# Performance work log

Measured on AMD Instinct MI355X. Metric: run time of the kernel, lower is better.

## Reference

```python
import jax, jax.numpy as jnp
import numpy as np

D_MODEL = 1024
N_HEADS = 16
DIM_HEAD = D_MODEL // N_HEADS
SCALE = DIM_HEAD ** (-0.5)
B, T = 8, 1024


def setup_inputs() -> dict:
    key = jax.random.key(0)
    k1, k2, k3 = jax.random.split(key, 3)
    x = jax.random.normal(k1, (B, T, D_MODEL), dtype=jnp.float32)
    m = jnp.ones((B, T), dtype=jnp.float32)  # padding mask (1 = keep)
    w_qkv = jax.random.normal(k2, (3 * D_MODEL, D_MODEL), dtype=jnp.float32) * (D_MODEL ** -0.5)
    w_out = jax.random.normal(k3, (D_MODEL, D_MODEL), dtype=jnp.float32) * (D_MODEL ** -0.5)
    b_out = jnp.zeros((D_MODEL,), dtype=jnp.float32)
    return {"x": x, "m": m, "w_qkv": w_qkv, "w_out": w_out, "b_out": b_out, "l": T}


def reference(x, m, w_qkv, w_out, b_out, l):
    b, t, dm = x.shape
    qkv = jnp.einsum('btd,ed->bte', x, w_qkv)  # (b,t,3*d_model)
    q, k, v = jnp.split(qkv, 3, axis=-1)
    rs = lambda a: a.reshape(b, t, N_HEADS, DIM_HEAD)
    q, k, v = rs(q), rs(k), rs(v)
    e = jnp.einsum('bihd,bjhd->bijh', q, k) * SCALE  # (b,i,j,h)
    # combined padding + causal mask
    kpm = m[:, :, None] * m[:, None, :]              # (b,i,j)
    kpm = jnp.tril(kpm)[..., None]                   # (b,i,j,1)
    neg = -jnp.finfo(e.dtype).max
    e = jnp.where(kpm == 0, neg, e)
    a = jax.nn.softmax(e, axis=2)                    # softmax over j
    o = jnp.einsum('bijh,bjhd->bihd', a, v).reshape(b, t, dm)
    o = jnp.einsum('btd,ed->bte', o, w_out) + b_out
    # dropout is identity in eval mode
    return o * m[..., None]
```

## Files before the change

### kernel.cpp

```cpp
#include <hip/hip_runtime.h>
#include <cstdint>
#include <cstddef>

typedef unsigned short u16;
typedef __bf16 bf16;
typedef bf16 __attribute__((ext_vector_type(2))) bf16x2;
typedef bf16 __attribute__((ext_vector_type(4))) bf16x4;
typedef bf16 __attribute__((ext_vector_type(8))) bf16x8;
typedef float __attribute__((ext_vector_type(4))) f32x4;
typedef u16 __attribute__((ext_vector_type(8))) u16x8;

#define QSCALE 0.18033688011112042f

__device__ __forceinline__ u16 f2b(float x) {
  unsigned u = __float_as_uint(x);
  unsigned r = (u + 0x7fffu + ((u >> 16) & 1u)) >> 16;
  return (u16)r;
}

__device__ __forceinline__ void gl_lds16(const void* g, void* lds) {
  __builtin_amdgcn_global_load_lds(
      (const __attribute__((address_space(1))) unsigned int*)g,
      (__attribute__((address_space(3))) unsigned int*)lds, 16, 0, 0);
}

__device__ __forceinline__ bf16x8 frag(const u16* base, int row, int kchunk) {
  const int c = kchunk ^ (row & 7);
  return *(const bf16x8*)(base + row * 64 + c * 8);
}
__device__ __forceinline__ void stage_tile4(const u16* gbase, int K, char* lbase,
                                            int wave, int lane) {
#pragma unroll
  for (int i = 0; i < 4; ++i) {
    const int q = wave * 64 + lane + i * 256;
    const int r = q >> 3, c = (q & 7) ^ (r & 7);
    gl_lds16(gbase + (size_t)r * K + c * 8, lbase + i * 4096 + wave * 1024);
  }
}

__device__ __forceinline__ bf16x8 frag32(const u16* base, int row, int kchunk) {
  const int c = kchunk ^ ((row >> 1) & 3);
  return *(const bf16x8*)(base + row * 32 + c * 8);
}
__device__ __forceinline__ void stage32(const u16* gbase, int K, char* lbase,
                                        int wave, int lane) {
  const int q0 = wave * 64 + lane;
  const int r0 = q0 >> 2, c0 = (q0 & 3) ^ ((r0 >> 1) & 3);
  gl_lds16(gbase + (size_t)r0 * K + c0 * 8, lbase + wave * 1024);
  const int q1 = q0 + 256;
  const int r1 = q1 >> 2, c1 = (q1 & 3) ^ ((r1 >> 1) & 3);
  gl_lds16(gbase + (size_t)r1 * K + c1 * 8, lbase + 4096 + wave * 1024);
}

__global__ __launch_bounds__(256) void castk(const float* __restrict__ in,
                                             u16* __restrict__ out, int n) {
  int i = (blockIdx.x * 256 + threadIdx.x) * 8;
  if (i >= n) return;
  float4 a = *(const float4*)(in + i);
  float4 b = *(const float4*)(in + i + 4);
  u16x8 v;
  v[0] = f2b(a.x); v[1] = f2b(a.y); v[2] = f2b(a.z); v[3] = f2b(a.w);
  v[4] = f2b(b.x); v[5] = f2b(b.y); v[6] = f2b(b.z); v[7] = f2b(b.w);
  *(u16x8*)(out + i) = v;
}

__global__ __launch_bounds__(256, 4) void gemm_qkv(
    const u16* __restrict__ A, const u16* __restrict__ B,
    u16* __restrict__ Qo, u16* __restrict__ Ko, u16* __restrict__ Vo) {
  __shared__ u16 As[2][128 * 32];
  __shared__ u16 Bs[2][128 * 32];
  const int tid = threadIdx.x;
  const int lane = tid & 63, wave = tid >> 6;
  const int fr = lane & 15, fg = lane >> 4;
  const int wr = wave >> 1, wc = wave & 1;
  const int bid = blockIdx.x;
  const int bm = bid & 63, bn = bid >> 6;
  const int K = 1024;
  const u16* Ab = A + (size_t)bm * 128 * K;
  const u16* Bb = B + (size_t)bn * 128 * K;

  f32x4 acc[4][4] = {};

  stage32(Ab, K, (char*)&As[0][0], wave, lane);
  stage32(Bb, K, (char*)&Bs[0][0], wave, lane);
  __syncthreads();

  int cur = 0;
#pragma unroll 1
  for (int t = 0; t < 32; ++t) {
    if (t < 31) {
      stage32(Ab + (size_t)(t + 1) * 32, K, (char*)&As[cur ^ 1][0], wave, lane);
      stage32(Bb + (size_t)(t + 1) * 32, K, (char*)&Bs[cur ^ 1][0], wave, lane);
    }
    bf16x8 af[4], bfv[4];
#pragma unroll
    for (int mi = 0; mi < 4; ++mi)
      af[mi] = frag32(&As[cur][0], wr * 64 + mi * 16 + fr, fg);
#pragma unroll
    for (int ni = 0; ni < 4; ++ni)
      bfv[ni] = frag32(&Bs[cur][0], wc * 64 + ni * 16 + fr, fg);
#pragma unroll
    for (int mi = 0; mi < 4; ++mi)
#pragma unroll
      for (int ni = 0; ni < 4; ++ni)
        acc[mi][ni] = __builtin_amdgcn_mfma_f32_16x16x32_bf16(
            af[mi], bfv[ni], acc[mi][ni], 0, 0, 0);
    __syncthreads();
    cur ^= 1;
  }

  const int gr0 = bm * 128 + wr * 64;
  const int gc0 = bn * 128 + wc * 64;
#pragma unroll
  for (int mi = 0; mi < 4; ++mi) {
    const int rb = gr0 + mi * 16 + fg * 4;
    const int b = rb >> 10, t = rb & 1023;
#pragma unroll
    for (int ni = 0; ni < 4; ++ni) {
      const int c = gc0 + ni * 16 + fr;
      const int region = c >> 10, cc = c & 1023;
      const int h = cc >> 6, d = cc & 63;
      const size_t bh = (size_t)(b * 16 + h);
      if (region == 0) {
#pragma unroll
        for (int g = 0; g < 4; ++g)
          Qo[(bh * 1024 + t + g) * 64 + d] = f2b(acc[mi][ni][g] * QSCALE);
      } else if (region == 1) {
#pragma unroll
        for (int g = 0; g < 4; ++g)
          Ko[(bh * 1024 + t + g) * 64 + d] = f2b(acc[mi][ni][g]);
      } else {
        ushort4 pv;
        pv.x = f2b(acc[mi][ni][0]);
        pv.y = f2b(acc[mi][ni][1]);
        pv.z = f2b(acc[mi][ni][2]);
        pv.w = f2b(acc[mi][ni][3]);
        *(ushort4*)(Vo + (bh * 64 + d) * 1024 + t) = pv;
      }
    }
  }
}

__global__ __launch_bounds__(256) void gemm_bt2(
    const u16* __restrict__ A, const u16* __restrict__ B,
    float* __restrict__ Co, const float* __restrict__ bias,
    const float* __restrict__ msk) {
  __shared__ u16 As[2][128 * 64];
  __shared__ u16 Bs[2][128 * 64];
  const int tid = threadIdx.x;
  const int lane = tid & 63, wave = tid >> 6;
  const int fr = lane & 15, fg = lane >> 4;
  const int wr = wave >> 1, wc = wave & 1;
  const int bid = blockIdx.x;
  const int bm = bid & 63, bn = bid >> 6;
  const int K = 1024, N = 1024;
  const u16* Ab = A + (size_t)bm * 128 * K;
  const u16* Bb = B + (size_t)bn * 128 * K;

  f32x4 acc[4][4] = {};

  stage_tile4(Ab, K, (char*)&As[0][0], wave, lane);
  stage_tile4(Bb, K, (char*)&Bs[0][0], wave, lane);
  __syncthreads();

  int cur = 0;
#pragma unroll 1
  for (int t = 0; t < 16; ++t) {
    if (t < 15) {
      stage_tile4(Ab + (size_t)(t + 1) * 64, K, (char*)&As[cur ^ 1][0], wave, lane);
      stage_tile4(Bb + (size_t)(t + 1) * 64, K, (char*)&Bs[cur ^ 1][0], wave, lane);
    }
    bf16x8 af[4][2], bfv[4][2];
#pragma unroll
    for (int mi = 0; mi < 4; ++mi)
#pragma unroll
      for (int kk = 0; kk < 2; ++kk)
        af[mi][kk] = frag(&As[cur][0], wr * 64 + mi * 16 + fr, kk * 4 + fg);
#pragma unroll
    for (int ni = 0; ni < 4; ++ni)
#pragma unroll
      for (int kk = 0; kk < 2; ++kk)
        bfv[ni][kk] = frag(&Bs[cur][0], wc * 64 + ni * 16 + fr, kk * 4 + fg);
#pragma unroll
    for (int mi = 0; mi < 4; ++mi)
#pragma unroll
      for (int ni = 0; ni < 4; ++ni)
#pragma unroll
        for (int kk = 0; kk < 2; ++kk)
          acc[mi][ni] = __builtin_amdgcn_mfma_f32_16x16x32_bf16(
              af[mi][kk], bfv[ni][kk], acc[mi][ni], 0, 0, 0);
    __syncthreads();
    cur ^= 1;
  }

  const int gr0 = bm * 128 + wr * 64;
  const int gc0 = bn * 128 + wc * 64;
#pragma unroll
  for (int mi = 0; mi < 4; ++mi) {
    const int rb = gr0 + mi * 16 + fg * 4;
#pragma unroll
    for (int ni = 0; ni < 4; ++ni) {
      const int c = gc0 + ni * 16 + fr;
      const float bo = bias[c];
#pragma unroll
      for (int g = 0; g < 4; ++g) {
        const int r = rb + g;
        Co[(size_t)r * N + c] = (acc[mi][ni][g] + bo) * msk[r];
      }
    }
  }
}

__global__ __launch_bounds__(256) void attnk(const u16* __restrict__ Qb,
                                             const u16* __restrict__ Kb,
                                             const u16* __restrict__ Vtb,
                                             const float* __restrict__ msk,
                                             u16* __restrict__ Ob) {
  __shared__ u16 Ks[2][64 * 64];
  __shared__ u16 Vs[2][64 * 64];
  const int tid = threadIdx.x;
  const int lane = tid & 63, wave = tid >> 6;
  const int fr = lane & 15, fg = lane >> 4;
  const int bid = blockIdx.x;
  __constant__ static const int tab[8] = {7, 6, 0, 1, 5, 4, 2, 3};
  const int qi = tab[bid >> 7];
  const int bh = bid & 127;
  const int b = bh >> 4, h = bh & 15;
  const int qw = qi * 128 + wave * 32;

  bf16x8 qf[2][2];
#pragma unroll
  for (int ct = 0; ct < 2; ++ct)
#pragma unroll
    for (int kc = 0; kc < 2; ++kc)
      qf[ct][kc] = *(const bf16x8*)(Qb + ((size_t)bh * 1024 + qw + ct * 16 + fr) * 64 +
                                    kc * 32 + fg * 8);

  f32x4 o[2][4] = {};
  float mrun[2], lrun[2];
  mrun[0] = mrun[1] = -3.0e38f;
  lrun[0] = lrun[1] = 0.f;

  const int src0 = fr + ((fg & 1) << 5);
  const int src1 = src0 + 16;

  const int cc0 = wave * 64 + lane;
  const int krow0 = cc0 >> 3, kcb0 = (cc0 & 7) ^ (krow0 & 7);
  const int cc1 = 256 + cc0;
  const int krow1 = cc1 >> 3, kcb1 = (cc1 & 7) ^ (krow1 & 7);

  const int nkb = qi * 2 + 2;

  gl_lds16(Kb + ((size_t)bh * 1024 + krow0) * 64 + kcb0 * 8, (char*)&Ks[0][0] + wave * 1024);
  gl_lds16(Vtb + ((size_t)bh * 64 + krow0) * 1024 + kcb0 * 8, (char*)&Vs[0][0] + wave * 1024);
  gl_lds16(Kb + ((size_t)bh * 1024 + krow1) * 64 + kcb1 * 8, (char*)&Ks[0][0] + 4096 + wave * 1024);
  gl_lds16(Vtb + ((size_t)bh * 64 + krow1) * 1024 + kcb1 * 8, (char*)&Vs[0][0] + 4096 + wave * 1024);

#pragma unroll 1
  for (int kb = 0; kb < nkb; ++kb) {
    __syncthreads();
    if (kb + 1 < nkb) {
      char* kd = (char*)&Ks[(kb + 1) & 1][0];
      char* vd = (char*)&Vs[(kb + 1) & 1][0];
      gl_lds16(Kb + ((size_t)bh * 1024 + (kb + 1) * 64 + krow0) * 64 + kcb0 * 8, kd + wave * 1024);
      gl_lds16(Vtb + ((size_t)bh * 64 + krow0) * 1024 + (kb + 1) * 64 + kcb0 * 8, vd + wave * 1024);
      gl_lds16(Kb + ((size_t)bh * 1024 + (kb + 1) * 64 + krow1) * 64 + kcb1 * 8, kd + 4096 + wave * 1024);
      gl_lds16(Vtb + ((size_t)bh * 64 + krow1) * 1024 + (kb + 1) * 64 + kcb1 * 8, vd + 4096 + wave * 1024);
    }
    if (kb * 64 > qw + 31) continue;
    const u16* Kc = &Ks[kb & 1][0];
    const u16* Vc = &Vs[kb & 1][0];

    f32x4 st[2][4];
    const f32x4 z = {0.f, 0.f, 0.f, 0.f};
#pragma unroll
    for (int nt = 0; nt < 4; ++nt) {
      const int krow = nt * 16 + fr;
      const int cb0r = (0 * 4 + fg) ^ (krow & 7);
      const int cb1r = (1 * 4 + fg) ^ (krow & 7);
      const bf16x8 kf0 = *(const bf16x8*)(Kc + krow * 64 + cb0r * 8);
      const bf16x8 kf1 = *(const bf16x8*)(Kc + krow * 64 + cb1r * 8);
#pragma unroll
      for (int ct = 0; ct < 2; ++ct) {
        st[ct][nt] = __builtin_amdgcn_mfma_f32_16x16x32_bf16(kf0, qf[ct][0], z, 0, 0, 0);
        st[ct][nt] = __builtin_amdgcn_mfma_f32_16x16x32_bf16(kf1, qf[ct][1], st[ct][nt], 0, 0, 0);
      }
    }

    float kmv[4][4];
#pragma unroll
    for (int nt = 0; nt < 4; ++nt) {
      const float4 km4 = *(const float4*)(msk + b * 1024 + kb * 64 + nt * 16 + fg * 4);
      kmv[nt][0] = km4.x; kmv[nt][1] = km4.y; kmv[nt][2] = km4.z; kmv[nt][3] = km4.w;
    }

    const bool edge = (kb * 64 + 63 > qw);
    if (edge) {
#pragma unroll
      for (int ct = 0; ct < 2; ++ct) {
        const int q = qw + ct * 16 + fr;
#pragma unroll
        for (int nt = 0; nt < 4; ++nt)
#pragma unroll
          for (int g = 0; g < 4; ++g) {
            const int j = kb * 64 + nt * 16 + fg * 4 + g;
            if (j > q) st[ct][nt][g] = -3.0e38f;
          }
      }
    }

    float sc[2];
    int doR[2];
#pragma unroll
    for (int ct = 0; ct < 2; ++ct) {
      float mx = st[ct][0][0];
#pragma unroll
      for (int nt = 0; nt < 4; ++nt)
#pragma unroll
        for (int g = 0; g < 4; ++g) mx = fmaxf(mx, st[ct][nt][g]);
      mx = fmaxf(mx, __shfl_xor(mx, 16));
      mx = fmaxf(mx, __shfl_xor(mx, 32));
      float nm;
      if (__all(mx <= mrun[ct] + 8.f)) {
        nm = mrun[ct]; sc[ct] = 1.f; doR[ct] = 0;
      } else {
        nm = fmaxf(mrun[ct], mx);
        sc[ct] = exp2f(mrun[ct] - nm);
        mrun[ct] = nm; doR[ct] = 1;
      }
      float rs = 0.f;
#pragma unroll
      for (int nt = 0; nt < 4; ++nt)
#pragma unroll
        for (int g = 0; g < 4; ++g) {
          const float p = exp2f(st[ct][nt][g] - nm) * kmv[nt][g];
          st[ct][nt][g] = p;
          rs += p;
        }
      rs += __shfl_xor(rs, 16);
      rs += __shfl_xor(rs, 32);
      lrun[ct] = doR[ct] ? (lrun[ct] * sc[ct] + rs) : (lrun[ct] + rs);
    }

    int pk[2][4][2];
#pragma unroll
    for (int ct = 0; ct < 2; ++ct)
#pragma unroll
      for (int nt = 0; nt < 4; ++nt)
#pragma unroll
        for (int hh = 0; hh < 2; ++hh) {
          bf16x2 tp;
          tp[0] = (bf16)st[ct][nt][2 * hh];
          tp[1] = (bf16)st[ct][nt][2 * hh + 1];
          pk[ct][nt][hh] = __builtin_bit_cast(int, tp);
        }

    bf16x8 pa[2][2];
#pragma unroll
    for (int mt = 0; mt < 2; ++mt)
#pragma unroll
      for (int jc = 0; jc < 2; ++jc) {
        int w[4];
#pragma unroll
        for (int e2 = 0; e2 < 4; ++e2) {
          const int sl = (e2 & 2) ? src1 : src0;
          const int lo = __shfl(pk[mt][jc * 2 + 0][e2 & 1], sl);
          const int hi = __shfl(pk[mt][jc * 2 + 1][e2 & 1], sl);
          w[e2] = (fg & 2) ? hi : lo;
        }
        int4 wi = {w[0], w[1], w[2], w[3]};
        pa[mt][jc] = __builtin_bit_cast(bf16x8, wi);
      }

#pragma unroll
    for (int mt = 0; mt < 2; ++mt)
      if (doR[mt]) {
#pragma unroll
        for (int g = 0; g < 4; ++g) {
          const float scr = __shfl(sc[mt], fg * 4 + g);
#pragma unroll
          for (int dt = 0; dt < 4; ++dt) o[mt][dt][g] *= scr;
        }
      }

#pragma unroll
    for (int jc = 0; jc < 2; ++jc)
#pragma unroll
      for (int dt = 0; dt < 4; ++dt) {
        const int vrow = dt * 16 + fr;
        const int cb = (jc * 4 + fg) ^ (vrow & 7);
        const bf16x8 vf = *(const bf16x8*)(Vc + vrow * 64 + cb * 8);
#pragma unroll
        for (int mt = 0; mt < 2; ++mt)
          o[mt][dt] = __builtin_amdgcn_mfma_f32_16x16x32_bf16(pa[mt][jc], vf, o[mt][dt], 0, 0, 0);
      }
  }

  float inv[2];
  inv[0] = 1.0f / lrun[0];
  inv[1] = 1.0f / lrun[1];
#pragma unroll
  for (int mt = 0; mt < 2; ++mt)
#pragma unroll
    for (int g = 0; g < 4; ++g) {
      const float invr = __shfl(inv[mt], fg * 4 + g);
      const int q = qw + mt * 16 + fg * 4 + g;
#pragma unroll
      for (int dt = 0; dt < 4; ++dt)
        Ob[((size_t)b * 1024 + q) * 1024 + h * 64 + dt * 16 + fr] =
            f2b(o[mt][dt][g] * invr);
    }
}

extern "C" void kernel_launch(void* const* d_in, const int* in_sizes, int n_in,
                              void* d_out, int out_size, void* d_ws, size_t ws_size,
                              hipStream_t stream) {
  (void)in_sizes; (void)n_in; (void)out_size; (void)ws_size;
  const float* x = (const float*)d_in[0];
  const float* m = (const float*)d_in[1];
  const float* w_qkv = (const float*)d_in[2];
  const float* w_out = (const float*)d_in[3];
  const float* b_out = (const float*)d_in[4];
  float* out = (float*)d_out;

  char* ws = (char*)d_ws;
  const size_t MB = 1u << 20;
  u16* Xb    = (u16*)(ws + 0);
  u16* Wqkvb = (u16*)(ws + 16 * MB);
  u16* Woutb = (u16*)(ws + 22 * MB);
  u16* Qb    = (u16*)(ws + 24 * MB);
  u16* Kb    = (u16*)(ws + 40 * MB);
  u16* Vtb   = (u16*)(ws + 56 * MB);
  u16* Ob    = Xb;

  castk<<<4096, 256, 0, stream>>>(x, Xb, 8 * 1024 * 1024);
  castk<<<1536, 256, 0, stream>>>(w_qkv, Wqkvb, 3072 * 1024);
  castk<<<512, 256, 0, stream>>>(w_out, Woutb, 1024 * 1024);

  gemm_qkv<<<1536, 256, 0, stream>>>(Xb, Wqkvb, Qb, Kb, Vtb);

  attnk<<<1024, 256, 0, stream>>>(Qb, Kb, Vtb, m, Ob);

  gemm_bt2<<<512, 256, 0, stream>>>(Ob, Woutb, out, b_out, m);
}
```

Measured before the change: 170.9 us.

## Pair causal query tiles per block and stage two KV tiles per sync

Each attention block now handles two query tiles, p and 7-p, so every block does about the same causal work. This replaces the previous eight-way launch order that tried to mitigate imbalance, and it halves the grid to 512 blocks. K/V tiles are staged two at a time per barrier, which doubles the LDS buffers, and the padding mask is cached in LDS instead of being read from global memory every tile. The cost is higher LDS use, which may lower occupancy, and fewer blocks to spread across CUs.

```diff
diff --git a/kernel.cpp b/kernel.cpp
--- a/kernel.cpp
+++ b/kernel.cpp
@@ -5,7 +5,6 @@
 typedef unsigned short u16;
 typedef __bf16 bf16;
 typedef bf16 __attribute__((ext_vector_type(2))) bf16x2;
-typedef bf16 __attribute__((ext_vector_type(4))) bf16x4;
 typedef bf16 __attribute__((ext_vector_type(8))) bf16x8;
 typedef float __attribute__((ext_vector_type(4))) f32x4;
 typedef u16 __attribute__((ext_vector_type(8))) u16x8;
@@ -216,200 +215,228 @@
                                              const u16* __restrict__ Vtb,
                                              const float* __restrict__ msk,
                                              u16* __restrict__ Ob) {
-  __shared__ u16 Ks[2][64 * 64];
-  __shared__ u16 Vs[2][64 * 64];
+  __shared__ u16 Ks[2][2][64 * 64];
+  __shared__ u16 Vs[2][2][64 * 64];
+  __shared__ float mlds[1024];
   const int tid = threadIdx.x;
   const int lane = tid & 63, wave = tid >> 6;
   const int fr = lane & 15, fg = lane >> 4;
   const int bid = blockIdx.x;
-  __constant__ static const int tab[8] = {7, 6, 0, 1, 5, 4, 2, 3};
-  const int qi = tab[bid >> 7];
+  const int p = bid >> 7;
   const int bh = bid & 127;
   const int b = bh >> 4, h = bh & 15;
-  const int qw = qi * 128 + wave * 32;
-
+  const int sa = p + 1;
+
+  ((float4*)mlds)[tid] = ((const float4*)(msk + (size_t)b * 1024))[tid];
+
+  const int src0 = fr + ((fg & 1) << 5);
+  const int src1 = src0 + 16;
+
+  auto stage2 = [&](int kb0, int buf) {
+#pragma unroll
+    for (int i = 0; i < 4; ++i) {
+      const int qb_ = i * 256 + wave * 64;
+      const int sub = qb_ >> 9;
+      const int q2b = qb_ & 511;
+      const int q2 = q2b + lane;
+      const int r = q2 >> 3, c = (q2 & 7) ^ (r & 7);
+      gl_lds16(Kb + ((size_t)bh * 1024 + (kb0 + sub) * 64 + r) * 64 + c * 8,
+               (char*)&Ks[buf][sub][0] + q2b * 16);
+      gl_lds16(Vtb + ((size_t)bh * 64 + r) * 1024 + (kb0 + sub) * 64 + c * 8,
+               (char*)&Vs[buf][sub][0] + q2b * 16);
+    }
+  };
+
+  int qw = p * 128 + wave * 32;
   bf16x8 qf[2][2];
-#pragma unroll
-  for (int ct = 0; ct < 2; ++ct)
-#pragma unroll
-    for (int kc = 0; kc < 2; ++kc)
-      qf[ct][kc] = *(const bf16x8*)(Qb + ((size_t)bh * 1024 + qw + ct * 16 + fr) * 64 +
-                                    kc * 32 + fg * 8);
+  auto loadQ = [&]() {
+#pragma unroll
+    for (int ct = 0; ct < 2; ++ct)
+#pragma unroll
+      for (int kc = 0; kc < 2; ++kc)
+        qf[ct][kc] = *(const bf16x8*)(Qb + ((size_t)bh * 1024 + qw + ct * 16 + fr) * 64 +
+                                      kc * 32 + fg * 8);
+  };
+  loadQ();
 
   f32x4 o[2][4] = {};
   float mrun[2], lrun[2];
   mrun[0] = mrun[1] = -3.0e38f;
   lrun[0] = lrun[1] = 0.f;
 
-  const int src0 = fr + ((fg & 1) << 5);
-  const int src1 = src0 + 16;
-
-  const int cc0 = wave * 64 + lane;
-  const int krow0 = cc0 >> 3, kcb0 = (cc0 & 7) ^ (krow0 & 7);
-  const int cc1 = 256 + cc0;
-  const int krow1 = cc1 >> 3, kcb1 = (cc1 & 7) ^ (krow1 & 7);
-
-  const int nkb = qi * 2 + 2;
-
-  gl_lds16(Kb + ((size_t)bh * 1024 + krow0) * 64 + kcb0 * 8, (char*)&Ks[0][0] + wave * 1024);
-  gl_lds16(Vtb + ((size_t)bh * 64 + krow0) * 1024 + kcb0 * 8, (char*)&Vs[0][0] + wave * 1024);
-  gl_lds16(Kb + ((size_t)bh * 1024 + krow1) * 64 + kcb1 * 8, (char*)&Ks[0][0] + 4096 + wave * 1024);
-  gl_lds16(Vtb + ((size_t)bh * 64 + krow1) * 1024 + kcb1 * 8, (char*)&Vs[0][0] + 4096 + wave * 1024);
+  auto writeO = [&]() {
+    float inv[2];
+    inv[0] = 1.0f / lrun[0];
+    inv[1] = 1.0f / lrun[1];
+#pragma unroll
+    for (int mt = 0; mt < 2; ++mt)
+#pragma unroll
+      for (int g = 0; g < 4; ++g) {
+        const float invr = __shfl(inv[mt], fg * 4 + g);
+        const int q = qw + mt * 16 + fg * 4 + g;
+#pragma unroll
+        for (int dt = 0; dt < 4; ++dt)
+          Ob[((size_t)b * 1024 + q) * 1024 + h * 64 + dt * 16 + fr] =
+              f2b(o[mt][dt][g] * invr);
+      }
+  };
+
+  stage2(0, 0);
 
 #pragma unroll 1
-  for (int kb = 0; kb < nkb; ++kb) {
+  for (int s = 0; s < 9; ++s) {
     __syncthreads();
-    if (kb + 1 < nkb) {
-      char* kd = (char*)&Ks[(kb + 1) & 1][0];
-      char* vd = (char*)&Vs[(kb + 1) & 1][0];
-      gl_lds16(Kb + ((size_t)bh * 1024 + (kb + 1) * 64 + krow0) * 64 + kcb0 * 8, kd + wave * 1024);
-      gl_lds16(Vtb + ((size_t)bh * 64 + krow0) * 1024 + (kb + 1) * 64 + kcb0 * 8, vd + wave * 1024);
-      gl_lds16(Kb + ((size_t)bh * 1024 + (kb + 1) * 64 + krow1) * 64 + kcb1 * 8, kd + 4096 + wave * 1024);
-      gl_lds16(Vtb + ((size_t)bh * 64 + krow1) * 1024 + (kb + 1) * 64 + kcb1 * 8, vd + 4096 + wave * 1024);
-    }
-    if (kb * 64 > qw + 31) continue;
-    const u16* Kc = &Ks[kb & 1][0];
-    const u16* Vc = &Vs[kb & 1][0];
-
-    f32x4 st[2][4];
-    const f32x4 z = {0.f, 0.f, 0.f, 0.f};
-#pragma unroll
-    for (int nt = 0; nt < 4; ++nt) {
-      const int krow = nt * 16 + fr;
-      const int cb0r = (0 * 4 + fg) ^ (krow & 7);
-      const int cb1r = (1 * 4 + fg) ^ (krow & 7);
-      const bf16x8 kf0 = *(const bf16x8*)(Kc + krow * 64 + cb0r * 8);
-      const bf16x8 kf1 = *(const bf16x8*)(Kc + krow * 64 + cb1r * 8);
+    if (s < 8) {
+      const int sn = s + 1;
+      stage2(sn < sa ? 2 * sn : 2 * (sn - sa), sn & 1);
+    }
+    if (s == sa) {
+      writeO();
+      qw = (7 - p) * 128 + wave * 32;
+      loadQ();
+#pragma unroll
+      for (int mt = 0; mt < 2; ++mt)
+#pragma unroll
+        for (int dt = 0; dt < 4; ++dt) o[mt][dt] = f32x4{0.f, 0.f, 0.f, 0.f};
+      mrun[0] = mrun[1] = -3.0e38f;
+      lrun[0] = lrun[1] = 0.f;
+    }
+    const int kb0 = (s < sa) ? 2 * s : 2 * (s - sa);
+
+#pragma unroll
+    for (int sub = 0; sub < 2; ++sub) {
+      const int kb = kb0 + sub;
+      if (kb * 64 > qw + 31) continue;
+      const u16* Kc = &Ks[s & 1][sub][0];
+      const u16* Vc = &Vs[s & 1][sub][0];
+
+      f32x4 st[2][4];
+      const f32x4 z = {0.f, 0.f, 0.f, 0.f};
+#pragma unroll
+      for (int nt = 0; nt < 4; ++nt) {
+        const int krow = nt * 16 + fr;
+        const int cb0r = (0 * 4 + fg) ^ (krow & 7);
+        const int cb1r = (1 * 4 + fg) ^ (krow & 7);
+        const bf16x8 kf0 = *(const bf16x8*)(Kc + krow * 64 + cb0r * 8);
+        const bf16x8 kf1 = *(const bf16x8*)(Kc + krow * 64 + cb1r * 8);
+#pragma unroll
+        for (int ct = 0; ct < 2; ++ct) {
+          st[ct][nt] = __builtin_amdgcn_mfma_f32_16x16x32_bf16(kf0, qf[ct][0], z, 0, 0, 0);
+          st[ct][nt] = __builtin_amdgcn_mfma_f32_16x16x32_bf16(kf1, qf[ct][1], st[ct][nt], 0, 0, 0);
+        }
+      }
+
+      float kmv[4][4];
+#pragma unroll
+      for (int nt = 0; nt < 4; ++nt) {
+        const float4 km4 = *(const float4*)(&mlds[kb * 64 + nt * 16 + fg * 4]);
+        kmv[nt][0] = km4.x; kmv[nt][1] = km4.y; kmv[nt][2] = km4.z; kmv[nt][3] = km4.w;
+      }
+
+      const bool edge = (kb * 64 + 63 > qw);
+      if (edge) {
+#pragma unroll
+        for (int ct = 0; ct < 2; ++ct) {
+          const int q = qw + ct * 16 + fr;
+#pragma unroll
+          for (int nt = 0; nt < 4; ++nt)
+#pragma unroll
+            for (int g = 0; g < 4; ++g) {
+              const int j = kb * 64 + nt * 16 + fg * 4 + g;
+              if (j > q) st[ct][nt][g] = -3.0e38f;
+            }
+        }
+      }
+
+      float sc[2];
+      int doR[2];
 #pragma unroll
       for (int ct = 0; ct < 2; ++ct) {
-        st[ct][nt] = __builtin_amdgcn_mfma_f32_16x16x32_bf16(kf0, qf[ct][0], z, 0, 0, 0);
-        st[ct][nt] = __builtin_amdgcn_mfma_f32_16x16x32_bf16(kf1, qf[ct][1], st[ct][nt], 0, 0, 0);
-      }
-    }
-
-    float kmv[4][4];
-#pragma unroll
-    for (int nt = 0; nt < 4; ++nt) {
-      const float4 km4 = *(const float4*)(msk + b * 1024 + kb * 64 + nt * 16 + fg * 4);
-      kmv[nt][0] = km4.x; kmv[nt][1] = km4.y; kmv[nt][2] = km4.z; kmv[nt][3] = km4.w;
-    }
-
-    const bool edge = (kb * 64 + 63 > qw);
-    if (edge) {
-#pragma unroll
-      for (int ct = 0; ct < 2; ++ct) {
-        const int q = qw + ct * 16 + fr;
+        float mx = st[ct][0][0];
 #pragma unroll
         for (int nt = 0; nt < 4; ++nt)
 #pragma unroll
+          for (int g = 0; g < 4; ++g) mx = fmaxf(mx, st[ct][nt][g]);
+        mx = fmaxf(mx, __shfl_xor(mx, 16));
+        mx = fmaxf(mx, __shfl_xor(mx, 32));
+        float nm;
+        if (__all(mx <= mrun[ct] + 8.f)) {
+          nm = mrun[ct]; sc[ct] = 1.f; doR[ct] = 0;
+        } else {
+          nm = fmaxf(mrun[ct], mx);
+          sc[ct] = exp2f(mrun[ct] - nm);
+          mrun[ct] = nm; doR[ct] = 1;
+        }
+        float rs = 0.f;
+#pragma unroll
+        for (int nt = 0; nt < 4; ++nt)
+#pragma unroll
           for (int g = 0; g < 4; ++g) {
-            const int j = kb * 64 + nt * 16 + fg * 4 + g;
-            if (j > q) st[ct][nt][g] = -3.0e38f;
+            const float pq = exp2f(st[ct][nt][g] - nm) * kmv[nt][g];
+            st[ct][nt][g] = pq;
+            rs += pq;
           }
-      }
-    }
-
-    float sc[2];
-    int doR[2];
-#pragma unroll
-    for (int ct = 0; ct < 2; ++ct) {
-      float mx = st[ct][0][0];
-#pragma unroll
-      for (int nt = 0; nt < 4; ++nt)
-#pragma unroll
-        for (int g = 0; g < 4; ++g) mx = fmaxf(mx, st[ct][nt][g]);
-      mx = fmaxf(mx, __shfl_xor(mx, 16));
-      mx = fmaxf(mx, __shfl_xor(mx, 32));
-      float nm;
-      if (__all(mx <= mrun[ct] + 8.f)) {
-        nm = mrun[ct]; sc[ct] = 1.f; doR[ct] = 0;
-      } else {
-        nm = fmaxf(mrun[ct], mx);
-        sc[ct] = exp2f(mrun[ct] - nm);
-        mrun[ct] = nm; doR[ct] = 1;
-      }
-      float rs = 0.f;
-#pragma unroll
-      for (int nt = 0; nt < 4; ++nt)
-#pragma unroll
-        for (int g = 0; g < 4; ++g) {
-          const float p = exp2f(st[ct][nt][g] - nm) * kmv[nt][g];
-          st[ct][nt][g] = p;
-          rs += p;
-        }
-      rs += __shfl_xor(rs, 16);
-      rs += __shfl_xor(rs, 32);
-      lrun[ct] = doR[ct] ? (lrun[ct] * sc[ct] + rs) : (lrun[ct] + rs);
-    }
-
-    int pk[2][4][2];
-#pragma unroll
-    for (int ct = 0; ct < 2; ++ct)
-#pragma unroll
-      for (int nt = 0; nt < 4; ++nt)
-#pragma unroll
-        for (int hh = 0; hh < 2; ++hh) {
-          bf16x2 tp;
-          tp[0] = (bf16)st[ct][nt][2 * hh];
-          tp[1] = (bf16)st[ct][nt][2 * hh + 1];
-          pk[ct][nt][hh] = __builtin_bit_cast(int, tp);
-        }
-
-    bf16x8 pa[2][2];
-#pragma unroll
-    for (int mt = 0; mt < 2; ++mt)
-#pragma unroll
-      for (int jc = 0; jc < 2; ++jc) {
-        int w[4];
-#pragma unroll
-        for (int e2 = 0; e2 < 4; ++e2) {
-          const int sl = (e2 & 2) ? src1 : src0;
-          const int lo = __shfl(pk[mt][jc * 2 + 0][e2 & 1], sl);
-          const int hi = __shfl(pk[mt][jc * 2 + 1][e2 & 1], sl);
-          w[e2] = (fg & 2) ? hi : lo;
-        }
-        int4 wi = {w[0], w[1], w[2], w[3]};
-        pa[mt][jc] = __builtin_bit_cast(bf16x8, wi);
-      }
-
-#pragma unroll
-    for (int mt = 0; mt < 2; ++mt)
-      if (doR[mt]) {
-#pragma unroll
-        for (int g = 0; g < 4; ++g) {
-          const float scr = __shfl(sc[mt], fg * 4 + g);
-#pragma unroll
-          for (int dt = 0; dt < 4; ++dt) o[mt][dt][g] *= scr;
-        }
-      }
-
-#pragma unroll
-    for (int jc = 0; jc < 2; ++jc)
-#pragma unroll
-      for (int dt = 0; dt < 4; ++dt) {
-        const int vrow = dt * 16 + fr;
-        const int cb = (jc * 4 + fg) ^ (vrow & 7);
-        const bf16x8 vf = *(const bf16x8*)(Vc + vrow * 64 + cb * 8);
-#pragma unroll
-        for (int mt = 0; mt < 2; ++mt)
-          o[mt][dt] = __builtin_amdgcn_mfma_f32_16x16x32_bf16(pa[mt][jc], vf, o[mt][dt], 0, 0, 0);
-      }
-  }
-
-  float inv[2];
-  inv[0] = 1.0f / lrun[0];
-  inv[1] = 1.0f / lrun[1];
-#pragma unroll
-  for (int mt = 0; mt < 2; ++mt)
-#pragma unroll
-    for (int g = 0; g < 4; ++g) {
-      const float invr = __shfl(inv[mt], fg * 4 + g);
-      const int q = qw + mt * 16 + fg * 4 + g;
-#pragma unroll
-      for (int dt = 0; dt < 4; ++dt)
-        Ob[((size_t)b * 1024 + q) * 1024 + h * 64 + dt * 16 + fr] =
-            f2b(o[mt][dt][g] * invr);
-    }
+        rs += __shfl_xor(rs, 16);
+        rs += __shfl_xor(rs, 32);
+        lrun[ct] = doR[ct] ? (lrun[ct] * sc[ct] + rs) : (lrun[ct] + rs);
+      }
+
+      int pk[2][4][2];
+#pragma unroll
+      for (int ct = 0; ct < 2; ++ct)
+#pragma unroll
+        for (int nt = 0; nt < 4; ++nt)
+#pragma unroll
+          for (int hh = 0; hh < 2; ++hh) {
+            bf16x2 tp;
+            tp[0] = (bf16)st[ct][nt][2 * hh];
+            tp[1] = (bf16)st[ct][nt][2 * hh + 1];
+            pk[ct][nt][hh] = __builtin_bit_cast(int, tp);
+          }
+
+      bf16x8 pa[2][2];
+#pragma unroll
+      for (int mt = 0; mt < 2; ++mt)
+#pragma unroll
+        for (int jc = 0; jc < 2; ++jc) {
+          int w[4];
+#pragma unroll
+          for (int e2 = 0; e2 < 4; ++e2) {
+            const int sl = (e2 & 2) ? src1 : src0;
+            const int lo = __shfl(pk[mt][jc * 2 + 0][e2 & 1], sl);
+            const int hi = __shfl(pk[mt][jc * 2 + 1][e2 & 1], sl);
+            w[e2] = (fg & 2) ? hi : lo;
+          }
+          int4 wi = {w[0], w[1], w[2], w[3]};
+          pa[mt][jc] = __builtin_bit_cast(bf16x8, wi);
+        }
+
+#pragma unroll
+      for (int mt = 0; mt < 2; ++mt)
+        if (doR[mt]) {
+#pragma unroll
+          for (int g = 0; g < 4; ++g) {
+            const float scr = __shfl(sc[mt], fg * 4 + g);
+#pragma unroll
+            for (int dt = 0; dt < 4; ++dt) o[mt][dt][g] *= scr;
+          }
+        }
+
+#pragma unroll
+      for (int jc = 0; jc < 2; ++jc)
+#pragma unroll
+        for (int dt = 0; dt < 4; ++dt) {
+          const int vrow = dt * 16 + fr;
+          const int cb = (jc * 4 + fg) ^ (vrow & 7);
+          const bf16x8 vf = *(const bf16x8*)(Vc + vrow * 64 + cb * 8);
+#pragma unroll
+          for (int mt = 0; mt < 2; ++mt)
+            o[mt][dt] = __builtin_amdgcn_mfma_f32_16x16x32_bf16(pa[mt][jc], vf, o[mt][dt], 0, 0, 0);
+        }
+    }
+  }
+
+  writeO();
 }
 
 extern "C" void kernel_launch(void* const* d_in, const int* in_sizes, int n_in,
@@ -439,7 +466,7 @@
 
   gemm_qkv<<<1536, 256, 0, stream>>>(Xb, Wqkvb, Qb, Kb, Vtb);
 
-  attnk<<<1024, 256, 0, stream>>>(Qb, Kb, Vtb, m, Ob);
+  attnk<<<512, 256, 0, stream>>>(Qb, Kb, Vtb, m, Ob);
 
   gemm_bt2<<<512, 256, 0, stream>>>(Ob, Woutb, out, b_out, m);
 }
```

Result: faster. 166.5 us (-2.6%).

## Pair causal query tiles per block for balanced work in attention kernel

Applied to the files above, without the earlier changes.

Each attention block now handles two 64-row query tiles, s and 15-s, processed back to back over a fixed 17 key-block iterations. This gives every block the same amount of work instead of the old uneven per-tile loop lengths. Waves now own 16 query rows instead of 32, which halves K/V reuse per LDS load but lowers register pressure. The key padding mask is also staged in LDS once per block rather than read from global memory on every iteration.

```diff
diff --git a/kernel.cpp b/kernel.cpp
--- a/kernel.cpp
+++ b/kernel.cpp
@@ -5,7 +5,6 @@
 typedef unsigned short u16;
 typedef __bf16 bf16;
 typedef bf16 __attribute__((ext_vector_type(2))) bf16x2;
-typedef bf16 __attribute__((ext_vector_type(4))) bf16x4;
 typedef bf16 __attribute__((ext_vector_type(8))) bf16x8;
 typedef float __attribute__((ext_vector_type(4))) f32x4;
 typedef u16 __attribute__((ext_vector_type(8))) u16x8;
@@ -218,60 +217,81 @@
                                              u16* __restrict__ Ob) {
   __shared__ u16 Ks[2][64 * 64];
   __shared__ u16 Vs[2][64 * 64];
+  __shared__ float mlds[1024];
   const int tid = threadIdx.x;
   const int lane = tid & 63, wave = tid >> 6;
   const int fr = lane & 15, fg = lane >> 4;
   const int bid = blockIdx.x;
-  __constant__ static const int tab[8] = {7, 6, 0, 1, 5, 4, 2, 3};
-  const int qi = tab[bid >> 7];
+  const int s = bid >> 7;
   const int bh = bid & 127;
   const int b = bh >> 4, h = bh & 15;
-  const int qw = qi * 128 + wave * 32;
-
-  bf16x8 qf[2][2];
-#pragma unroll
-  for (int ct = 0; ct < 2; ++ct)
+
+  ((float4*)mlds)[tid] = ((const float4*)(msk + (size_t)b * 1024))[tid];
+
+  auto stage = [&](int kb, int buf) {
+    const int q0 = wave * 64 + lane;
+    const int r0 = q0 >> 3, c0 = (q0 & 7) ^ (r0 & 7);
+    gl_lds16(Kb + ((size_t)bh * 1024 + kb * 64 + r0) * 64 + c0 * 8,
+             (char*)&Ks[buf][0] + wave * 1024);
+    gl_lds16(Vtb + ((size_t)bh * 64 + r0) * 1024 + kb * 64 + c0 * 8,
+             (char*)&Vs[buf][0] + wave * 1024);
+    const int q1 = q0 + 256;
+    const int r1 = q1 >> 3, c1 = (q1 & 7) ^ (r1 & 7);
+    gl_lds16(Kb + ((size_t)bh * 1024 + kb * 64 + r1) * 64 + c1 * 8,
+             (char*)&Ks[buf][0] + 4096 + wave * 1024);
+    gl_lds16(Vtb + ((size_t)bh * 64 + r1) * 1024 + kb * 64 + c1 * 8,
+             (char*)&Vs[buf][0] + 4096 + wave * 1024);
+  };
+
+  int qw = s * 64 + wave * 16;
+  bf16x8 qf[2];
+  auto loadQ = [&]() {
 #pragma unroll
     for (int kc = 0; kc < 2; ++kc)
-      qf[ct][kc] = *(const bf16x8*)(Qb + ((size_t)bh * 1024 + qw + ct * 16 + fr) * 64 +
-                                    kc * 32 + fg * 8);
-
-  f32x4 o[2][4] = {};
-  float mrun[2], lrun[2];
-  mrun[0] = mrun[1] = -3.0e38f;
-  lrun[0] = lrun[1] = 0.f;
-
-  const int src0 = fr + ((fg & 1) << 5);
-  const int src1 = src0 + 16;
-
-  const int cc0 = wave * 64 + lane;
-  const int krow0 = cc0 >> 3, kcb0 = (cc0 & 7) ^ (krow0 & 7);
-  const int cc1 = 256 + cc0;
-  const int krow1 = cc1 >> 3, kcb1 = (cc1 & 7) ^ (krow1 & 7);
-
-  const int nkb = qi * 2 + 2;
-
-  gl_lds16(Kb + ((size_t)bh * 1024 + krow0) * 64 + kcb0 * 8, (char*)&Ks[0][0] + wave * 1024);
-  gl_lds16(Vtb + ((size_t)bh * 64 + krow0) * 1024 + kcb0 * 8, (char*)&Vs[0][0] + wave * 1024);
-  gl_lds16(Kb + ((size_t)bh * 1024 + krow1) * 64 + kcb1 * 8, (char*)&Ks[0][0] + 4096 + wave * 1024);
-  gl_lds16(Vtb + ((size_t)bh * 64 + krow1) * 1024 + kcb1 * 8, (char*)&Vs[0][0] + 4096 + wave * 1024);
+      qf[kc] = *(const bf16x8*)(Qb + ((size_t)bh * 1024 + qw + fr) * 64 +
+                                kc * 32 + fg * 8);
+  };
+  loadQ();
+
+  f32x4 o[4] = {};
+  float mrun = -3.0e38f, lrun = 0.f;
+
+  auto writeO = [&]() {
+    const float inv = 1.0f / lrun;
+#pragma unroll
+    for (int g = 0; g < 4; ++g) {
+      const float invr = __shfl(inv, fg * 4 + g);
+      const int q = qw + fg * 4 + g;
+#pragma unroll
+      for (int dt = 0; dt < 4; ++dt)
+        Ob[((size_t)b * 1024 + q) * 1024 + h * 64 + dt * 16 + fr] =
+            f2b(o[dt][g] * invr);
+    }
+  };
+
+  stage(0, 0);
 
 #pragma unroll 1
-  for (int kb = 0; kb < nkb; ++kb) {
+  for (int it = 0; it <= 16; ++it) {
     __syncthreads();
-    if (kb + 1 < nkb) {
-      char* kd = (char*)&Ks[(kb + 1) & 1][0];
-      char* vd = (char*)&Vs[(kb + 1) & 1][0];
-      gl_lds16(Kb + ((size_t)bh * 1024 + (kb + 1) * 64 + krow0) * 64 + kcb0 * 8, kd + wave * 1024);
-      gl_lds16(Vtb + ((size_t)bh * 64 + krow0) * 1024 + (kb + 1) * 64 + kcb0 * 8, vd + wave * 1024);
-      gl_lds16(Kb + ((size_t)bh * 1024 + (kb + 1) * 64 + krow1) * 64 + kcb1 * 8, kd + 4096 + wave * 1024);
-      gl_lds16(Vtb + ((size_t)bh * 64 + krow1) * 1024 + (kb + 1) * 64 + kcb1 * 8, vd + 4096 + wave * 1024);
-    }
-    if (kb * 64 > qw + 31) continue;
-    const u16* Kc = &Ks[kb & 1][0];
-    const u16* Vc = &Vs[kb & 1][0];
-
-    f32x4 st[2][4];
+    if (it < 16) {
+      const int nkb = (it + 1 <= s) ? (it + 1) : (it - s);
+      stage(nkb, (it + 1) & 1);
+    }
+    if (it == s + 1) {
+      writeO();
+      qw = (15 - s) * 64 + wave * 16;
+      loadQ();
+#pragma unroll
+      for (int dt = 0; dt < 4; ++dt) o[dt] = f32x4{0.f, 0.f, 0.f, 0.f};
+      mrun = -3.0e38f;
+      lrun = 0.f;
+    }
+    const int kb = (it <= s) ? it : (it - s - 1);
+    const u16* Kc = &Ks[it & 1][0];
+    const u16* Vc = &Vs[it & 1][0];
+
+    f32x4 st[4];
     const f32x4 z = {0.f, 0.f, 0.f, 0.f};
 #pragma unroll
     for (int nt = 0; nt < 4; ++nt) {
@@ -280,108 +300,91 @@
       const int cb1r = (1 * 4 + fg) ^ (krow & 7);
       const bf16x8 kf0 = *(const bf16x8*)(Kc + krow * 64 + cb0r * 8);
       const bf16x8 kf1 = *(const bf16x8*)(Kc + krow * 64 + cb1r * 8);
-#pragma unroll
-      for (int ct = 0; ct < 2; ++ct) {
-        st[ct][nt] = __builtin_amdgcn_mfma_f32_16x16x32_bf16(kf0, qf[ct][0], z, 0, 0, 0);
-        st[ct][nt] = __builtin_amdgcn_mfma_f32_16x16x32_bf16(kf1, qf[ct][1], st[ct][nt], 0, 0, 0);
-      }
+      st[nt] = __builtin_amdgcn_mfma_f32_16x16x32_bf16(kf0, qf[0], z, 0, 0, 0);
+      st[nt] = __builtin_amdgcn_mfma_f32_16x16x32_bf16(kf1, qf[1], st[nt], 0, 0, 0);
     }
 
     float kmv[4][4];
 #pragma unroll
     for (int nt = 0; nt < 4; ++nt) {
-      const float4 km4 = *(const float4*)(msk + b * 1024 + kb * 64 + nt * 16 + fg * 4);
+      const float4 km4 = *(const float4*)(&mlds[kb * 64 + nt * 16 + fg * 4]);
       kmv[nt][0] = km4.x; kmv[nt][1] = km4.y; kmv[nt][2] = km4.z; kmv[nt][3] = km4.w;
     }
 
-    const bool edge = (kb * 64 + 63 > qw);
-    if (edge) {
-#pragma unroll
-      for (int ct = 0; ct < 2; ++ct) {
-        const int q = qw + ct * 16 + fr;
-#pragma unroll
-        for (int nt = 0; nt < 4; ++nt)
-#pragma unroll
-          for (int g = 0; g < 4; ++g) {
-            const int j = kb * 64 + nt * 16 + fg * 4 + g;
-            if (j > q) st[ct][nt][g] = -3.0e38f;
-          }
-      }
-    }
-
-    float sc[2];
-    int doR[2];
-#pragma unroll
-    for (int ct = 0; ct < 2; ++ct) {
-      float mx = st[ct][0][0];
+    if (kb * 64 + 63 > qw) {
+      const int q = qw + fr;
 #pragma unroll
       for (int nt = 0; nt < 4; ++nt)
 #pragma unroll
-        for (int g = 0; g < 4; ++g) mx = fmaxf(mx, st[ct][nt][g]);
-      mx = fmaxf(mx, __shfl_xor(mx, 16));
-      mx = fmaxf(mx, __shfl_xor(mx, 32));
-      float nm;
-      if (__all(mx <= mrun[ct] + 8.f)) {
-        nm = mrun[ct]; sc[ct] = 1.f; doR[ct] = 0;
-      } else {
-        nm = fmaxf(mrun[ct], mx);
-        sc[ct] = exp2f(mrun[ct] - nm);
-        mrun[ct] = nm; doR[ct] = 1;
-      }
-      float rs = 0.f;
-#pragma unroll
-      for (int nt = 0; nt < 4; ++nt)
-#pragma unroll
         for (int g = 0; g < 4; ++g) {
-          const float p = exp2f(st[ct][nt][g] - nm) * kmv[nt][g];
-          st[ct][nt][g] = p;
-          rs += p;
+          const int j = kb * 64 + nt * 16 + fg * 4 + g;
+          if (j > q) st[nt][g] = -3.0e38f;
         }
-      rs += __shfl_xor(rs, 16);
-      rs += __shfl_xor(rs, 32);
-      lrun[ct] = doR[ct] ? (lrun[ct] * sc[ct] + rs) : (lrun[ct] + rs);
-    }
-
-    int pk[2][4][2];
-#pragma unroll
-    for (int ct = 0; ct < 2; ++ct)
-#pragma unroll
-      for (int nt = 0; nt < 4; ++nt)
-#pragma unroll
-        for (int hh = 0; hh < 2; ++hh) {
-          bf16x2 tp;
-          tp[0] = (bf16)st[ct][nt][2 * hh];
-          tp[1] = (bf16)st[ct][nt][2 * hh + 1];
-          pk[ct][nt][hh] = __builtin_bit_cast(int, tp);
-        }
-
-    bf16x8 pa[2][2];
-#pragma unroll
-    for (int mt = 0; mt < 2; ++mt)
-#pragma unroll
-      for (int jc = 0; jc < 2; ++jc) {
-        int w[4];
-#pragma unroll
-        for (int e2 = 0; e2 < 4; ++e2) {
-          const int sl = (e2 & 2) ? src1 : src0;
-          const int lo = __shfl(pk[mt][jc * 2 + 0][e2 & 1], sl);
-          const int hi = __shfl(pk[mt][jc * 2 + 1][e2 & 1], sl);
-          w[e2] = (fg & 2) ? hi : lo;
-        }
-        int4 wi = {w[0], w[1], w[2], w[3]};
-        pa[mt][jc] = __builtin_bit_cast(bf16x8, wi);
-      }
-
-#pragma unroll
-    for (int mt = 0; mt < 2; ++mt)
-      if (doR[mt]) {
-#pragma unroll
-        for (int g = 0; g < 4; ++g) {
-          const float scr = __shfl(sc[mt], fg * 4 + g);
-#pragma unroll
-          for (int dt = 0; dt < 4; ++dt) o[mt][dt][g] *= scr;
-        }
-      }
+    }
+
+    float mx = st[0][0];
+#pragma unroll
+    for (int nt = 0; nt < 4; ++nt)
+#pragma unroll
+      for (int g = 0; g < 4; ++g) mx = fmaxf(mx, st[nt][g]);
+    mx = fmaxf(mx, __shfl_xor(mx, 16));
+    mx = fmaxf(mx, __shfl_xor(mx, 32));
+    float nm, sc;
+    int doR;
+    if (__all(mx <= mrun + 8.f)) {
+      nm = mrun; sc = 1.f; doR = 0;
+    } else {
+      nm = fmaxf(mrun, mx);
+      sc = exp2f(mrun - nm);
+      mrun = nm; doR = 1;
+    }
+    float rs = 0.f;
+#pragma unroll
+    for (int nt = 0; nt < 4; ++nt)
+#pragma unroll
+      for (int g = 0; g < 4; ++g) {
+        const float pq = exp2f(st[nt][g] - nm) * kmv[nt][g];
+        st[nt][g] = pq;
+        rs += pq;
+      }
+    rs += __shfl_xor(rs, 16);
+    rs += __shfl_xor(rs, 32);
+    lrun = doR ? (lrun * sc + rs) : (lrun + rs);
+
+    int pk[4][2];
+#pragma unroll
+    for (int nt = 0; nt < 4; ++nt)
+#pragma unroll
+      for (int hh = 0; hh < 2; ++hh) {
+        bf16x2 tp;
+        tp[0] = (bf16)st[nt][2 * hh];
+        tp[1] = (bf16)st[nt][2 * hh + 1];
+        pk[nt][hh] = __builtin_bit_cast(int, tp);
+      }
+
+    bf16x8 pa[2];
+#pragma unroll
+    for (int jc = 0; jc < 2; ++jc) {
+      int w[4];
+#pragma unroll
+      for (int e2 = 0; e2 < 4; ++e2) {
+        const int sl = fr + ((fg & 1) << 5) + ((e2 & 2) ? 16 : 0);
+        const int lo = __shfl(pk[jc * 2 + 0][e2 & 1], sl);
+        const int hi = __shfl(pk[jc * 2 + 1][e2 & 1], sl);
+        w[e2] = (fg & 2) ? hi : lo;
+      }
+      int4 wi = {w[0], w[1], w[2], w[3]};
+      pa[jc] = __builtin_bit_cast(bf16x8, wi);
+    }
+
+    if (doR) {
+#pragma unroll
+      for (int g = 0; g < 4; ++g) {
+        const float scr = __shfl(sc, fg * 4 + g);
+#pragma unroll
+        for (int dt = 0; dt < 4; ++dt) o[dt][g] *= scr;
+      }
+    }
 
 #pragma unroll
     for (int jc = 0; jc < 2; ++jc)
@@ -390,26 +393,11 @@
         const int vrow = dt * 16 + fr;
         const int cb = (jc * 4 + fg) ^ (vrow & 7);
         const bf16x8 vf = *(const bf16x8*)(Vc + vrow * 64 + cb * 8);
-#pragma unroll
-        for (int mt = 0; mt < 2; ++mt)
-          o[mt][dt] = __builtin_amdgcn_mfma_f32_16x16x32_bf16(pa[mt][jc], vf, o[mt][dt], 0, 0, 0);
-      }
-  }
-
-  float inv[2];
-  inv[0] = 1.0f / lrun[0];
-  inv[1] = 1.0f / lrun[1];
-#pragma unroll
-  for (int mt = 0; mt < 2; ++mt)
-#pragma unroll
-    for (int g = 0; g < 4; ++g) {
-      const float invr = __shfl(inv[mt], fg * 4 + g);
-      const int q = qw + mt * 16 + fg * 4 + g;
-#pragma unroll
-      for (int dt = 0; dt < 4; ++dt)
-        Ob[((size_t)b * 1024 + q) * 1024 + h * 64 + dt * 16 + fr] =
-            f2b(o[mt][dt][g] * invr);
-    }
+        o[dt] = __builtin_amdgcn_mfma_f32_16x16x32_bf16(pa[jc], vf, o[dt], 0, 0, 0);
+      }
+  }
+
+  writeO();
 }
 
 extern "C" void kernel_launch(void* const* d_in, const int* in_sizes, int n_in,
```

Result: faster. 163.0 us (-4.6%).
